# Optimization experiments

Hardware: AMD Instinct MI355X
Metric: run time of the kernel (lower is better)

The kernel has to match this reference:

```python
import jax, jax.numpy as jnp
import numpy as np

B = 16384
F = 256  # num_features
H1, H2 = 64, 32  # hidden_units


def setup_inputs() -> dict:
    key = jax.random.key(0)
    kx, k1, kb1, k2, kb2, k3, kb3 = jax.random.split(key, 7)
    x = jax.random.normal(kx, (B, F), dtype=jnp.float32)
    # Stacked per-feature MLP params (torch Linear-style fan-in init scale).
    W1 = jax.random.normal(k1, (F, 1, H1), dtype=jnp.float32) * 1.0      # fan_in=1
    b1 = jax.random.normal(kb1, (F, H1), dtype=jnp.float32) * 0.1
    W2 = jax.random.normal(k2, (F, H1, H2), dtype=jnp.float32) * (1.0 / np.sqrt(H1))
    b2 = jax.random.normal(kb2, (F, H2), dtype=jnp.float32) * 0.1
    W3 = jax.random.normal(k3, (F, H2, 1), dtype=jnp.float32) * (1.0 / np.sqrt(H2))
    b3 = jax.random.normal(kb3, (F, 1), dtype=jnp.float32) * 0.1
    bias = jnp.zeros((1,), dtype=jnp.float32)
    return {"x": x, "W1": W1, "b1": b1, "W2": W2, "b2": b2,
            "W3": W3, "b3": b3, "bias": bias}


def reference(x, W1, b1, W2, b2, W3, b3, bias):
    # All F independent 1->64->32->1 MLPs batched as grouped GEMMs.
    # Layer 1: input dim is 1, so it's an outer-product broadcast.
    h1 = jax.nn.relu(x[:, :, None] * W1[:, 0, :] + b1)          # [B, F, H1]
    h2 = jax.nn.relu(jnp.einsum('bfh,fhk->bfk', h1, W2) + b2)   # [B, F, H2]
    contributions = jnp.einsum('bfk,fko->bfo', h2, W3)[..., 0] + b3[:, 0]  # [B, F]
    logits = bias[0] + contributions.sum(axis=1)                # [B]
    probs = jax.nn.sigmoid(logits)
    return logits, probs
```

## Files before the change

### kernel.cpp

```cpp
#include <hip/hip_runtime.h>
#include <math.h>


#define NAM_B   16384
#define NAM_F   256
#define SPLITS  16
#define RPS     (NAM_B / SPLITS)
#define TILES   (RPS / 16)
#define NGRP    8

typedef __attribute__((ext_vector_type(8))) _Float16 f16x8;
typedef __attribute__((ext_vector_type(4))) _Float16 f16x4;
typedef __attribute__((ext_vector_type(2))) _Float16 f16x2;
typedef __attribute__((ext_vector_type(4))) float    f32x4;

__global__ __launch_bounds__(256) void nam_xt(const float* __restrict__ x,
                                              _Float16* __restrict__ xT) {
    __shared__ float xs[64][65];
    const int t  = threadIdx.x;
    const int r0 = (blockIdx.x & 255) * 64;
    const int c0 = (blockIdx.x >> 8) * 64;
    const int rr = t >> 4;
    const int cc = (t & 15) * 4;
    #pragma unroll
    for (int e = 0; e < 4; ++e) {
        const float4 v = *reinterpret_cast<const float4*>(
            x + (size_t)(r0 + rr + e*16) * NAM_F + c0 + cc);
        xs[rr + e*16][cc+0] = v.x; xs[rr + e*16][cc+1] = v.y;
        xs[rr + e*16][cc+2] = v.z; xs[rr + e*16][cc+3] = v.w;
    }
    __syncthreads();
    const int wc = t >> 4;
    const int j  = (t & 15) * 4;
    #pragma unroll
    for (int e = 0; e < 4; ++e) {
        const int c = wc + e*16;
        f16x4 o = {(_Float16)xs[j+0][c], (_Float16)xs[j+1][c],
                   (_Float16)xs[j+2][c], (_Float16)xs[j+3][c]};
        *reinterpret_cast<f16x4*>(xT + (size_t)(c0 + c) * NAM_B + r0 + j) = o;
    }
}

__global__ __launch_bounds__(256) void nam_w2p(const float* __restrict__ W2,
                                               _Float16* __restrict__ w2p) {
    const int f = blockIdx.x;
    const int t = threadIdx.x;
    const int s = t >> 7, a = (t >> 6) & 1, L = t & 63;
    const int hi = L >> 4, m = L & 15;
    const float* __restrict__ W2f = W2 + (size_t)f * (64*32);
    f16x8 o;
    #pragma unroll
    for (int j = 0; j < 8; ++j)
        o[j] = (_Float16)W2f[(s*32 + hi*8 + j)*32 + a*16 + m];
    *reinterpret_cast<f16x8*>(w2p + ((size_t)((f*2 + s)*2 + a)*64 + L) * 8) = o;
}

__global__ __launch_bounds__(256, 4) void nam_main(
    const float* __restrict__ W1, const float* __restrict__ b1,
    const float* __restrict__ b2, const float* __restrict__ W3,
    const _Float16* __restrict__ xT, const _Float16* __restrict__ w2p,
    float* __restrict__ partial) {
    const int t    = threadIdx.x;
    const int w    = t >> 6, lane = t & 63;
    const int f     = (blockIdx.x & 63) * 4 + w;
    const int split = blockIdx.x >> 6;
    const int hi = lane >> 4, m = lane & 15;

    const f16x8* __restrict__ wp8 = reinterpret_cast<const f16x8*>(w2p);
    const size_t fb = (size_t)f * 4 * 64;
    const f16x8 a_s0a0 = wp8[fb + 0*64 + lane];
    const f16x8 a_s0a1 = wp8[fb + 1*64 + lane];
    const f16x8 a_s1a0 = wp8[fb + 2*64 + lane];
    const f16x8 a_s1a1 = wp8[fb + 3*64 + lane];

    const float* __restrict__ w1f = W1 + f * 64;
    const float* __restrict__ b1f = b1 + f * 64;
    f16x2 w1h[8], b1h[8];
    #pragma unroll
    for (int s = 0; s < 2; ++s)
        #pragma unroll
        for (int u = 0; u < 4; ++u) {
            const int h = s*32 + hi*8 + 2*u;
            w1h[s*4+u] = (f16x2){(_Float16)w1f[h], (_Float16)w1f[h+1]};
            b1h[s*4+u] = (f16x2){(_Float16)b1f[h], (_Float16)b1f[h+1]};
        }
    const f32x4 b2v0 = *reinterpret_cast<const f32x4*>(b2 + f*32 + hi*4);
    const f32x4 b2v1 = *reinterpret_cast<const f32x4*>(b2 + f*32 + 16 + hi*4);
    const f32x4 w3v0 = *reinterpret_cast<const f32x4*>(W3 + f*32 + hi*4);
    const f32x4 w3v1 = *reinterpret_cast<const f32x4*>(W3 + f*32 + 16 + hi*4);

    const _Float16* __restrict__ xcol = xT + (size_t)f * NAM_B + split * RPS + m;
    float* __restrict__ pout = partial + (size_t)(f & 7) * NAM_B + split * RPS;

    _Float16 xc = xcol[0];
    const f16x2 hzero = {(_Float16)0.f, (_Float16)0.f};
    for (int tl = 0; tl < TILES; ++tl) {
        const int pf = (tl + 1 < TILES) ? (tl + 1) * 16 : 0;
        const _Float16 xn = xcol[pf];
        const f16x2 xb = {xc, xc};
        union { f16x2 h[4]; f16x8 v; } bf0, bf1;
        #pragma unroll
        for (int u = 0; u < 4; ++u) {
            bf0.h[u] = __builtin_elementwise_max(xb * w1h[u]     + b1h[u],     hzero);
            bf1.h[u] = __builtin_elementwise_max(xb * w1h[4 + u] + b1h[4 + u], hzero);
        }
        f32x4 acc0 = __builtin_amdgcn_mfma_f32_16x16x32_f16(a_s0a0, bf0.v, b2v0, 0,0,0);
        acc0       = __builtin_amdgcn_mfma_f32_16x16x32_f16(a_s1a0, bf1.v, acc0, 0,0,0);
        f32x4 acc1 = __builtin_amdgcn_mfma_f32_16x16x32_f16(a_s0a1, bf0.v, b2v1, 0,0,0);
        acc1       = __builtin_amdgcn_mfma_f32_16x16x32_f16(a_s1a1, bf1.v, acc1, 0,0,0);
        float ts = 0.f;
        #pragma unroll
        for (int r = 0; r < 4; ++r) {
            ts = fmaf(fmaxf(acc0[r], 0.f), w3v0[r], ts);
            ts = fmaf(fmaxf(acc1[r], 0.f), w3v1[r], ts);
        }
        ts += __shfl_xor(ts, 16);
        ts += __shfl_xor(ts, 32);
        if (hi == 0) atomicAdd(pout + tl*16 + m, ts);
        xc = xn;
    }
}

__global__ __launch_bounds__(256) void nam_phase2(
    const float* __restrict__ partial, const float* __restrict__ b3,
    const float* __restrict__ bias, float* __restrict__ out) {
    __shared__ float red[4];
    const int t = threadIdx.x;
    float v = b3[t];
    #pragma unroll
    for (int off = 32; off; off >>= 1) v += __shfl_xor(v, off);
    if ((t & 63) == 0) red[t >> 6] = v;
    __syncthreads();
    const float sb3 = red[0] + red[1] + red[2] + red[3];
    const int b = blockIdx.x * 256 + t;
    float s = bias[0] + sb3;
    #pragma unroll
    for (int g = 0; g < NGRP; ++g) s += partial[(size_t)g * NAM_B + b];
    out[b] = s;
    out[NAM_B + b] = 1.0f / (1.0f + expf(-s));
}

extern "C" void kernel_launch(void* const* d_in, const int* in_sizes, int n_in,
                              void* d_out, int out_size, void* d_ws, size_t ws_size,
                              hipStream_t stream) {
    const float* x    = (const float*)d_in[0];
    const float* W1   = (const float*)d_in[1];
    const float* b1   = (const float*)d_in[2];
    const float* W2   = (const float*)d_in[3];
    const float* b2   = (const float*)d_in[4];
    const float* W3   = (const float*)d_in[5];
    const float* b3   = (const float*)d_in[6];
    const float* bias = (const float*)d_in[7];
    float* out = (float*)d_out;

    float*    partial = (float*)d_ws;
    _Float16* xT  = (_Float16*)((char*)d_ws + (size_t)NGRP * NAM_B * 4);
    _Float16* w2p = (_Float16*)((char*)d_ws + (size_t)NGRP * NAM_B * 4
                                            + (size_t)NAM_F * NAM_B * 2);

    hipMemsetAsync(partial, 0, (size_t)NGRP * NAM_B * 4, stream);
    nam_xt  <<<dim3(1024), 256, 0, stream>>>(x, xT);
    nam_w2p <<<dim3(NAM_F), 256, 0, stream>>>(W2, w2p);
    nam_main<<<dim3(1024), 256, 0, stream>>>(W1, b1, b2, W3, xT, w2p, partial);
    nam_phase2<<<dim3(NAM_B / 256), 256, 0, stream>>>(partial, b3, bias, out);
}
```

Before: 125.0 us.

## Merge prep kernels with memset and double batch splits in main kernel

Folds the x transpose, the W2 repacking and the zeroing of the partial buffer into one prep kernel, so a memset and a launch are removed. The batch is split into 32 chunks instead of 16, giving twice as many blocks for the main kernel, and the launch bound is raised to 8 blocks per CU. The main loop is unrolled by 2 and its prefetch clamp is dropped, so the last iteration reads one tile past the split's range; for the final split this runs into the next feature's column, or past the end of xT for the last feature, where it lands in the w2p workspace. Smaller per-block work means fewer loop iterations to hide latency and more atomics per output, traded against higher occupancy.

```diff
diff --git a/kernel.cpp b/kernel.cpp
--- a/kernel.cpp
+++ b/kernel.cpp
@@ -4,7 +4,7 @@
 
 #define NAM_B   16384
 #define NAM_F   256
-#define SPLITS  16
+#define SPLITS  32
 #define RPS     (NAM_B / SPLITS)
 #define TILES   (RPS / 16)
 #define NGRP    8
@@ -14,48 +14,55 @@
 typedef __attribute__((ext_vector_type(2))) _Float16 f16x2;
 typedef __attribute__((ext_vector_type(4))) float    f32x4;
 
-__global__ __launch_bounds__(256) void nam_xt(const float* __restrict__ x,
-                                              _Float16* __restrict__ xT) {
+__global__ __launch_bounds__(256) void nam_prep(
+    const float* __restrict__ x, const float* __restrict__ W2,
+    _Float16* __restrict__ xT, _Float16* __restrict__ w2p,
+    float* __restrict__ partial) {
     __shared__ float xs[64][65];
-    const int t  = threadIdx.x;
-    const int r0 = (blockIdx.x & 255) * 64;
-    const int c0 = (blockIdx.x >> 8) * 64;
-    const int rr = t >> 4;
-    const int cc = (t & 15) * 4;
-    #pragma unroll
-    for (int e = 0; e < 4; ++e) {
-        const float4 v = *reinterpret_cast<const float4*>(
-            x + (size_t)(r0 + rr + e*16) * NAM_F + c0 + cc);
-        xs[rr + e*16][cc+0] = v.x; xs[rr + e*16][cc+1] = v.y;
-        xs[rr + e*16][cc+2] = v.z; xs[rr + e*16][cc+3] = v.w;
-    }
-    __syncthreads();
-    const int wc = t >> 4;
-    const int j  = (t & 15) * 4;
-    #pragma unroll
-    for (int e = 0; e < 4; ++e) {
-        const int c = wc + e*16;
-        f16x4 o = {(_Float16)xs[j+0][c], (_Float16)xs[j+1][c],
-                   (_Float16)xs[j+2][c], (_Float16)xs[j+3][c]};
-        *reinterpret_cast<f16x4*>(xT + (size_t)(c0 + c) * NAM_B + r0 + j) = o;
+    const int b = blockIdx.x;
+    const int t = threadIdx.x;
+    if (b < 1024) {
+        const int r0 = (b & 255) * 64;
+        const int c0 = (b >> 8) * 64;
+        const int rr = t >> 4;
+        const int cc = (t & 15) * 4;
+        #pragma unroll
+        for (int e = 0; e < 4; ++e) {
+            const float4 v = *reinterpret_cast<const float4*>(
+                x + (size_t)(r0 + rr + e*16) * NAM_F + c0 + cc);
+            xs[rr + e*16][cc+0] = v.x; xs[rr + e*16][cc+1] = v.y;
+            xs[rr + e*16][cc+2] = v.z; xs[rr + e*16][cc+3] = v.w;
+        }
+        __syncthreads();
+        const int wc = t >> 4;
+        const int j  = (t & 15) * 4;
+        #pragma unroll
+        for (int e = 0; e < 4; ++e) {
+            const int c = wc + e*16;
+            f16x4 o = {(_Float16)xs[j+0][c], (_Float16)xs[j+1][c],
+                       (_Float16)xs[j+2][c], (_Float16)xs[j+3][c]};
+            *reinterpret_cast<f16x4*>(xT + (size_t)(c0 + c) * NAM_B + r0 + j) = o;
+        }
+    } else if (b < 1280) {
+        const int f = b - 1024;
+        const int s = t >> 7, a = (t >> 6) & 1, L = t & 63;
+        const int hi = L >> 4, m = L & 15;
+        const float* __restrict__ W2f = W2 + (size_t)f * (64*32);
+        f16x8 o;
+        #pragma unroll
+        for (int j = 0; j < 8; ++j)
+            o[j] = (_Float16)W2f[(s*32 + hi*8 + j)*32 + a*16 + m];
+        *reinterpret_cast<f16x8*>(w2p + ((size_t)((f*2 + s)*2 + a)*64 + L) * 8) = o;
+    } else {
+        const int i = (b - 1280) * 256 + t;
+        float4* p4 = reinterpret_cast<float4*>(partial);
+        #pragma unroll
+        for (int e = 0; e < 8; ++e)
+            p4[(size_t)i * 8 + e] = make_float4(0.f, 0.f, 0.f, 0.f);
     }
 }
 
-__global__ __launch_bounds__(256) void nam_w2p(const float* __restrict__ W2,
-                                               _Float16* __restrict__ w2p) {
-    const int f = blockIdx.x;
-    const int t = threadIdx.x;
-    const int s = t >> 7, a = (t >> 6) & 1, L = t & 63;
-    const int hi = L >> 4, m = L & 15;
-    const float* __restrict__ W2f = W2 + (size_t)f * (64*32);
-    f16x8 o;
-    #pragma unroll
-    for (int j = 0; j < 8; ++j)
-        o[j] = (_Float16)W2f[(s*32 + hi*8 + j)*32 + a*16 + m];
-    *reinterpret_cast<f16x8*>(w2p + ((size_t)((f*2 + s)*2 + a)*64 + L) * 8) = o;
-}
-
-__global__ __launch_bounds__(256, 4) void nam_main(
+__global__ __launch_bounds__(256, 8) void nam_main(
     const float* __restrict__ W1, const float* __restrict__ b1,
     const float* __restrict__ b2, const float* __restrict__ W3,
     const _Float16* __restrict__ xT, const _Float16* __restrict__ w2p,
@@ -94,9 +101,9 @@
 
     _Float16 xc = xcol[0];
     const f16x2 hzero = {(_Float16)0.f, (_Float16)0.f};
+    #pragma unroll 2
     for (int tl = 0; tl < TILES; ++tl) {
-        const int pf = (tl + 1 < TILES) ? (tl + 1) * 16 : 0;
-        const _Float16 xn = xcol[pf];
+        const _Float16 xn = xcol[(tl + 1) * 16];
         const f16x2 xb = {xc, xc};
         union { f16x2 h[4]; f16x8 v; } bf0, bf1;
         #pragma unroll
@@ -158,9 +165,7 @@
     _Float16* w2p = (_Float16*)((char*)d_ws + (size_t)NGRP * NAM_B * 4
                                             + (size_t)NAM_F * NAM_B * 2);
 
-    hipMemsetAsync(partial, 0, (size_t)NGRP * NAM_B * 4, stream);
-    nam_xt  <<<dim3(1024), 256, 0, stream>>>(x, xT);
-    nam_w2p <<<dim3(NAM_F), 256, 0, stream>>>(W2, w2p);
-    nam_main<<<dim3(1024), 256, 0, stream>>>(W1, b1, b2, W3, xT, w2p, partial);
+    nam_prep<<<dim3(1296), 256, 0, stream>>>(x, W2, xT, w2p, partial);
+    nam_main<<<dim3(SPLITS * 64), 256, 0, stream>>>(W1, b1, b2, W3, xT, w2p, partial);
     nam_phase2<<<dim3(NAM_B / 256), 256, 0, stream>>>(partial, b3, bias, out);
 }
```

New measurement: 187.0 us. +49.7%, slower.
